# Kernel optimization log

Hardware: AMD Instinct MI355X
Metric: run time of the kernel (lower is better)

The kernel has to match this reference:

```python
import jax, jax.numpy as jnp
import numpy as np


def setup_inputs() -> dict:
    key = jax.random.key(0)
    k1, k2 = jax.random.split(key)
    B, T, D = 32, 1024, 384
    encodings = jax.random.normal(k1, (B, T, D), dtype=jnp.float32)
    durations = jax.random.randint(k2, (B, T), 0, 8, dtype=jnp.int32)
    return {"encodings": encodings, "durations": durations}


def reference(encodings, durations):
    # encodings: [B, T, D] float; durations: [B, T] int (torch code rounds .item())
    B, T, D = encodings.shape
    reps = jnp.round(durations).astype(jnp.int32)            # [B, T]
    csum = jnp.cumsum(reps, axis=1)                          # [B, T] exclusive end offsets
    totals = csum[:, -1]                                     # [B] expanded length per batch
    # max_len computed from concrete durations (dynamic output length, like the torch code)
    max_len = int(jnp.max(totals))
    pos = jnp.arange(max_len)                                # [L]
    # frame p belongs to token j where csum[j-1] <= p < csum[j] -> searchsorted right
    idx = jax.vmap(lambda c: jnp.searchsorted(c, pos, side="right"))(csum)  # [B, L]
    idx = jnp.minimum(idx, T - 1)
    out = jnp.take_along_axis(encodings, idx[:, :, None], axis=1)           # [B, L, D]
    mask = pos[None, :] < totals[:, None]                                   # [B, L]
    return jnp.where(mask[:, :, None], out, jnp.zeros((), dtype=encodings.dtype))
```

## Files before the change

### kernel.cpp

```cpp
#include <hip/hip_runtime.h>

#define NB 32
#define NT 1024
#define ND 384
#define ND4 (ND / 4)
#define THREADS 256
#define ILP 8
#define CHUNK (THREADS * ILP)

typedef float vfloat4 __attribute__((ext_vector_type(4)));

__global__ void __launch_bounds__(NT)
scan_scatter_kernel(const int* __restrict__ dur,
                    int* __restrict__ idx,
                    int* __restrict__ totals,
                    int max_len) {
    __shared__ int wsum[16];
    const int b = blockIdx.x;
    const int t = threadIdx.x;
    const int lane = t & 63;
    const int w = t >> 6;
    const int d = dur[b * NT + t];

    int x = d;
    #pragma unroll
    for (int off = 1; off < 64; off <<= 1) {
        int y = __shfl_up(x, off, 64);
        if (lane >= off) x += y;
    }
    if (lane == 63) wsum[w] = x;
    __syncthreads();
    if (w == 0) {
        int v = (lane < 16) ? wsum[lane] : 0;
        #pragma unroll
        for (int off = 1; off < 16; off <<= 1) {
            int y = __shfl_up(v, off, 64);
            if (lane >= off) v += y;
        }
        if (lane < 16) wsum[lane] = v;
    }
    __syncthreads();
    const int csum_t = x + (w ? wsum[w - 1] : 0);
    const int total  = wsum[15];

    int* idx_b = idx + (size_t)b * max_len;
    for (int p = csum_t - d; p < csum_t; ++p)
        idx_b[p] = t;
    for (int p = total + t; p < max_len; p += NT)
        idx_b[p] = 0;
    if (t == NT - 1)
        totals[b] = total;
}

__global__ void __launch_bounds__(THREADS)
gather_kernel(const vfloat4* __restrict__ enc,
              const int* __restrict__ idx,
              const int* __restrict__ totals,
              vfloat4* __restrict__ out,
              int max_len, int f4_per_batch) {
    const int b = blockIdx.y;
    const int total_f4 = totals[b] * ND4;
    const int* idx_b = idx + (size_t)b * max_len;
    const vfloat4* enc_b = enc + (size_t)b * NT * ND4;
    vfloat4* out_b = out + (size_t)b * (size_t)max_len * ND4;

    const int base = blockIdx.x * CHUNK + threadIdx.x;

    int j[ILP], t[ILP], d4[ILP];
    #pragma unroll
    for (int k = 0; k < ILP; ++k) {
        j[k] = base + k * THREADS;
        const int jc = j[k] < f4_per_batch ? j[k] : f4_per_batch - 1;
        const int p  = jc / ND4;
        d4[k] = jc - p * ND4;
        t[k]  = idx_b[p];
    }
    vfloat4 v[ILP];
    #pragma unroll
    for (int k = 0; k < ILP; ++k)
        v[k] = enc_b[(size_t)t[k] * ND4 + d4[k]];
    #pragma unroll
    for (int k = 0; k < ILP; ++k) {
        if (j[k] >= total_f4)
            v[k] = (vfloat4){0.f, 0.f, 0.f, 0.f};
        if (j[k] < f4_per_batch)
            __builtin_nontemporal_store(v[k], &out_b[j[k]]);
    }
}

extern "C" void kernel_launch(void* const* d_in, const int* in_sizes, int n_in,
                              void* d_out, int out_size, void* d_ws, size_t ws_size,
                              hipStream_t stream) {
    const float* enc = (const float*)d_in[0];
    const int*   dur = (const int*)d_in[1];
    float* out = (float*)d_out;

    const int max_len = out_size / (NB * ND);

    int* totals = (int*)d_ws;
    int* idx    = totals + NB;

    scan_scatter_kernel<<<NB, NT, 0, stream>>>(dur, idx, totals, max_len);

    const int f4pb = max_len * ND4;
    const int blocks_x = (f4pb + CHUNK - 1) / CHUNK;
    dim3 grid(blocks_x, NB);
    gather_kernel<<<grid, THREADS, 0, stream>>>(
        (const vfloat4*)enc, idx, totals, (vfloat4*)out, max_len, f4pb);
}
```

Measured before the change: 222.1 us.

## Replace per-frame gather with per-token scatter expansion and fused zero padding

Instead of building a frame-to-token index and gathering each output frame, each wavefront now reads one token row of encodings once and writes it to all of its duration frames. The scan kernel stores the cumulative sums and also writes the zero padding past each batch's total length. This removes the index array round trip and the per-element divide and index lookups, and each input row is read only once. In exchange, the amount of work per wave depends on the durations, which can unbalance the load. The padding stores also run inside only 32 blocks.

```diff
diff --git a/kernel.cpp b/kernel.cpp
--- a/kernel.cpp
+++ b/kernel.cpp
@@ -4,17 +4,17 @@
 #define NT 1024
 #define ND 384
 #define ND4 (ND / 4)
-#define THREADS 256
-#define ILP 8
-#define CHUNK (THREADS * ILP)
+#define FPW 4
+#define WPB 4
+#define FPB (FPW * WPB)
 
 typedef float vfloat4 __attribute__((ext_vector_type(4)));
 
 __global__ void __launch_bounds__(NT)
-scan_scatter_kernel(const int* __restrict__ dur,
-                    int* __restrict__ idx,
-                    int* __restrict__ totals,
-                    int max_len) {
+scan_pad_kernel(const int* __restrict__ dur,
+                int* __restrict__ csum,
+                vfloat4* __restrict__ out,
+                int max_len) {
     __shared__ int wsum[16];
     const int b = blockIdx.x;
     const int t = threadIdx.x;
@@ -40,51 +40,56 @@
         if (lane < 16) wsum[lane] = v;
     }
     __syncthreads();
-    const int csum_t = x + (w ? wsum[w - 1] : 0);
-    const int total  = wsum[15];
+    const int c = x + (w ? wsum[w - 1] : 0);
+    const int total = wsum[15];
+    csum[b * NT + t] = c;
 
-    int* idx_b = idx + (size_t)b * max_len;
-    for (int p = csum_t - d; p < csum_t; ++p)
-        idx_b[p] = t;
-    for (int p = total + t; p < max_len; p += NT)
-        idx_b[p] = 0;
-    if (t == NT - 1)
-        totals[b] = total;
+    vfloat4* out_b = out + (size_t)b * max_len * ND4;
+    const vfloat4 z = {0.f, 0.f, 0.f, 0.f};
+    const int end = max_len * ND4;
+    for (int i = total * ND4 + t; i < end; i += NT)
+        __builtin_nontemporal_store(z, &out_b[i]);
 }
 
-__global__ void __launch_bounds__(THREADS)
-gather_kernel(const vfloat4* __restrict__ enc,
-              const int* __restrict__ idx,
-              const int* __restrict__ totals,
+__global__ void __launch_bounds__(256)
+expand_kernel(const vfloat4* __restrict__ enc,
+              const int* __restrict__ csum,
               vfloat4* __restrict__ out,
-              int max_len, int f4_per_batch) {
+              int max_len) {
     const int b = blockIdx.y;
-    const int total_f4 = totals[b] * ND4;
-    const int* idx_b = idx + (size_t)b * max_len;
+    const int lane = threadIdx.x & 63;
+    const int wv = threadIdx.x >> 6;
+    const int f0 = blockIdx.x * FPB + wv * FPW;
+
+    const int* csum_b = csum + b * NT;
     const vfloat4* enc_b = enc + (size_t)b * NT * ND4;
     vfloat4* out_b = out + (size_t)b * (size_t)max_len * ND4;
 
-    const int base = blockIdx.x * CHUNK + threadIdx.x;
+    int e[FPW], s[FPW];
+    #pragma unroll
+    for (int k = 0; k < FPW; ++k)
+        e[k] = csum_b[f0 + k];
+    s[0] = f0 ? csum_b[f0 - 1] : 0;
+    #pragma unroll
+    for (int k = 1; k < FPW; ++k)
+        s[k] = e[k - 1];
 
-    int j[ILP], t[ILP], d4[ILP];
+    vfloat4 v0[FPW], v1[FPW];
     #pragma unroll
-    for (int k = 0; k < ILP; ++k) {
-        j[k] = base + k * THREADS;
-        const int jc = j[k] < f4_per_batch ? j[k] : f4_per_batch - 1;
-        const int p  = jc / ND4;
-        d4[k] = jc - p * ND4;
-        t[k]  = idx_b[p];
+    for (int k = 0; k < FPW; ++k) {
+        const vfloat4* src = enc_b + (size_t)(f0 + k) * ND4;
+        v0[k] = src[lane];
+        if (lane < 32) v1[k] = src[64 + lane];
     }
-    vfloat4 v[ILP];
+
     #pragma unroll
-    for (int k = 0; k < ILP; ++k)
-        v[k] = enc_b[(size_t)t[k] * ND4 + d4[k]];
-    #pragma unroll
-    for (int k = 0; k < ILP; ++k) {
-        if (j[k] >= total_f4)
-            v[k] = (vfloat4){0.f, 0.f, 0.f, 0.f};
-        if (j[k] < f4_per_batch)
-            __builtin_nontemporal_store(v[k], &out_b[j[k]]);
+    for (int k = 0; k < FPW; ++k) {
+        for (int p = s[k]; p < e[k]; ++p) {
+            vfloat4* dst = out_b + (size_t)p * ND4;
+            __builtin_nontemporal_store(v0[k], dst + lane);
+            if (lane < 32)
+                __builtin_nontemporal_store(v1[k], dst + 64 + lane);
+        }
     }
 }
 
@@ -97,14 +102,11 @@
 
     const int max_len = out_size / (NB * ND);
 
-    int* totals = (int*)d_ws;
-    int* idx    = totals + NB;
+    int* csum = (int*)d_ws;
 
-    scan_scatter_kernel<<<NB, NT, 0, stream>>>(dur, idx, totals, max_len);
+    scan_pad_kernel<<<NB, NT, 0, stream>>>(dur, csum, (vfloat4*)out, max_len);
 
-    const int f4pb = max_len * ND4;
-    const int blocks_x = (f4pb + CHUNK - 1) / CHUNK;
-    dim3 grid(blocks_x, NB);
-    gather_kernel<<<grid, THREADS, 0, stream>>>(
-        (const vfloat4*)enc, idx, totals, (vfloat4*)out, max_len, f4pb);
+    dim3 grid(NT / FPB, NB);
+    expand_kernel<<<grid, 256, 0, stream>>>(
+        (const vfloat4*)enc, csum, (vfloat4*)out, max_len);
 }
```

Measured after the change: 225.2 us. Within noise of the previous version (+1.4%).
